# Optimization experiments

Measured on AMD Instinct MI355X. Metric: run time of the kernel, lower is better.

Reference implementation:

```python
import jax, jax.numpy as jnp
import numpy as np

N_NODES = 100000


def _add_self_loops(edge_index, n):
    loop = jnp.arange(n, dtype=edge_index.dtype)
    src = jnp.concatenate([edge_index[0], loop])
    dst = jnp.concatenate([edge_index[1], loop])
    return src, dst


def _gcn_conv(x, W, b, src, dst, n):
    # h = X W, then symmetric-normalized scatter-add over edges (PyG GCNConv)
    h = x @ W
    ones = jnp.ones(src.shape[0], dtype=h.dtype)
    deg = jax.ops.segment_sum(ones, dst, num_segments=n)  # in-degree incl. self loops
    dinv = jnp.where(deg > 0, jax.lax.rsqrt(deg), 0.0)
    norm = dinv[src] * dinv[dst]                           # [E]
    msg = h[src] * norm[:, None]                           # gather + scale
    out = jax.ops.segment_sum(msg, dst, num_segments=n)    # scatter-add
    return out + b


def setup_inputs() -> dict:
    key = jax.random.key(0)
    k1, k2, k3, k4 = jax.random.split(key, 4)
    F, H, C = 128, 128, 16
    x = jax.random.normal(k1, (N_NODES, F), dtype=jnp.float32)
    edge_index = jax.random.randint(k2, (2, 1600000), 0, N_NODES, dtype=jnp.int64)
    W1 = jax.random.normal(k3, (F, H), dtype=jnp.float32) / np.sqrt(F)
    b1 = jnp.zeros((H,), dtype=jnp.float32)
    W2 = jax.random.normal(k4, (H, C), dtype=jnp.float32) / np.sqrt(H)
    b2 = jnp.zeros((C,), dtype=jnp.float32)
    return {"x": x, "edge_index": edge_index, "W1": W1, "b1": b1, "W2": W2, "b2": b2}


def reference(x, edge_index, W1, b1, W2, b2):
    n = x.shape[0]
    src, dst = _add_self_loops(edge_index, n)
    h = _gcn_conv(x, W1, b1, src, dst, n)
    h = jax.nn.relu(h)
    # dropout(p=0.1) treated as identity (deterministic eval-mode reference)
    logits = _gcn_conv(h, W2, b2, src, dst, n)
    return logits, jax.nn.log_softmax(logits, axis=1)
```

## Files before the change

### kernel.cpp

```cpp
#include <hip/hip_runtime.h>
#include <math.h>


#define ELLW 72
#define EPB 16384
#define BSH 9
#define MAXEB 100
#define MAXBK 200

typedef __attribute__((ext_vector_type(8))) short short8;
typedef __attribute__((ext_vector_type(4))) float f32x4;

__device__ __forceinline__ float bf2f(unsigned short u) {
    return __uint_as_float(((unsigned int)u) << 16);
}
__device__ __forceinline__ unsigned short f2bf(float f) {
    unsigned int u = __float_as_uint(f);
    unsigned int r = (u + 0x7fffu + ((u >> 16) & 1u)) >> 16;
    return (unsigned short)r;
}

__global__ void k_prep(unsigned short* __restrict__ h, float* __restrict__ g,
                       const float* __restrict__ W1, unsigned short* __restrict__ wt,
                       int n) {
    int i = blockIdx.x * blockDim.x + threadIdx.x;
    if (i < 16384) {
        int nc = i >> 7, k = i & 127;
        wt[i] = f2bf(W1[k * 128 + nc]);
    }
    if (i < 128) h[(size_t)n * 128 + i] = 0;
    if (i < 16) g[(size_t)n * 16 + i] = 0.f;
}

__global__ void k_hist(const int* __restrict__ dst, int E,
                       int* __restrict__ hist, int nbuck) {
    __shared__ int lh[MAXBK];
    const int t = threadIdx.x, blk = blockIdx.x;
    for (int i = t; i < nbuck; i += 256) lh[i] = 0;
    __syncthreads();
    const int e0 = blk * EPB;
    const int e1 = min(e0 + EPB, E);
    for (int e = e0 + t; e < e1; e += 256)
        atomicAdd(&lh[dst[e] >> BSH], 1);
    __syncthreads();
    for (int i = t; i < nbuck; i += 256)
        hist[blk * nbuck + i] = lh[i];
}

__global__ void k_scan(int* __restrict__ hist, int* __restrict__ bstart,
                       int* __restrict__ bcount, int neb, int nbuck) {
    __shared__ unsigned short lh[MAXEB * MAXBK];
    __shared__ int sc[256];
    const int t = threadIdx.x;
    const int items = neb * nbuck;
    for (int i = t; i < items; i += 256) lh[i] = (unsigned short)hist[i];
    __syncthreads();
    int total = 0;
    if (t < nbuck)
        for (int blk = 0; blk < neb; ++blk) total += lh[blk * nbuck + t];
    sc[t] = total;
    __syncthreads();
    for (int o = 1; o < 256; o <<= 1) {
        int x = 0;
        if (t >= o) x = sc[t - o];
        __syncthreads();
        if (t >= o) sc[t] += x;
        __syncthreads();
    }
    if (t < nbuck) {
        int run = sc[t] - total;
        bstart[t] = run;
        bcount[t] = total;
        for (int blk = 0; blk < neb; ++blk) {
            int idx = blk * nbuck + t;
            int v = lh[idx];
            hist[idx] = run;
            run += v;
        }
    }
}

__global__ void k_bin(const int* __restrict__ src, const int* __restrict__ dst, int E,
                      const int* __restrict__ hist, int* __restrict__ binned, int nbuck) {
    __shared__ int cnt[MAXBK];
    const int t = threadIdx.x, blk = blockIdx.x;
    for (int i = t; i < nbuck; i += 256) cnt[i] = hist[blk * nbuck + i];
    __syncthreads();
    const int e0 = blk * EPB;
    const int e1 = min(e0 + EPB, E);
    for (int e = e0 + t; e < e1; e += 256) {
        int d = dst[e];
        int b = d >> BSH;
        int pos = atomicAdd(&cnt[b], 1);
        binned[pos] = src[e] | ((d & ((1 << BSH) - 1)) << 17);
    }
}

__global__ void k_ell(const int* __restrict__ binned, const int* __restrict__ bstart,
                      const int* __restrict__ bcount, int* __restrict__ deg,
                      int* __restrict__ col, int n) {
    __shared__ int ldeg[1 << BSH];
    const int t = threadIdx.x, b = blockIdx.x;
    const int node0 = b << BSH;
    for (int i = t; i < (1 << BSH); i += 256) ldeg[i] = 0;
    __syncthreads();
    const int st = bstart[b], cv = bcount[b];
    for (int i = t; i < cv; i += 256) {
        int v = binned[st + i];
        int s = v & 0x1FFFF;
        int dl = v >> 17;
        int q = atomicAdd(&ldeg[dl], 1);
        if (q < ELLW) col[(size_t)(node0 + dl) * ELLW + q] = s;
    }
    __syncthreads();
    for (int i = t; i < (1 << BSH); i += 256) {
        int node = node0 + i;
        if (node < n) {
            int dgv = ldeg[i];
            deg[node] = dgv;
            int dc = dgv > ELLW ? ELLW : dgv;
            int kend = (dc + 7) & ~7;
            for (int q = dc; q < kend; ++q) col[(size_t)node * ELLW + q] = n;
        }
    }
}

__global__ void k_gemm1(const float* __restrict__ x, const unsigned short* __restrict__ wt,
                        const int* __restrict__ deg, unsigned short* __restrict__ h,
                        int n) {
    __shared__ unsigned short xs[64 * 136];
    const int t = threadIdx.x;
    const int row0 = blockIdx.x * 64;
    for (int i = t; i < 2048; i += 256) {
        int r = i >> 5, c4 = (i & 31) << 2;
        int gr = row0 + r;
        float4 v = make_float4(0.f, 0.f, 0.f, 0.f);
        if (gr < n) v = *(const float4*)(x + (size_t)gr * 128 + c4);
        ushort4 u;
        u.x = f2bf(v.x); u.y = f2bf(v.y); u.z = f2bf(v.z); u.w = f2bf(v.w);
        *(ushort4*)(xs + r * 136 + c4) = u;
    }
    __syncthreads();
    const int w = t >> 6;
    const int lane = t & 63;
    const int m = lane & 15, q = lane >> 4;
    f32x4 acc[8];
#pragma unroll
    for (int ns = 0; ns < 8; ++ns) acc[ns] = (f32x4){0.f, 0.f, 0.f, 0.f};
#pragma unroll
    for (int kt = 0; kt < 4; ++kt) {
        short8 a = *(const short8*)(xs + (w * 16 + m) * 136 + kt * 32 + q * 8);
#pragma unroll
        for (int ns = 0; ns < 8; ++ns) {
            short8 b = *(const short8*)((const short*)wt + (ns * 16 + m) * 128 + kt * 32 + q * 8);
            acc[ns] = __builtin_amdgcn_mfma_f32_16x16x32_bf16(a, b, acc[ns], 0, 0, 0);
        }
    }
    unsigned short* xsw = xs + (w * 16) * 136;
    float srow[4];
#pragma unroll
    for (int reg = 0; reg < 4; ++reg) {
        int gr = row0 + w * 16 + q * 4 + reg;
        srow[reg] = (gr < n) ? rsqrtf((float)(deg[gr] + 1)) : 0.f;
    }
#pragma unroll
    for (int ns = 0; ns < 8; ++ns)
#pragma unroll
        for (int reg = 0; reg < 4; ++reg)
            xsw[(q * 4 + reg) * 136 + ns * 16 + m] = f2bf(acc[ns][reg] * srow[reg]);
    __syncthreads();
#pragma unroll
    for (int it = 0; it < 8; ++it) {
        int rl = (lane >> 5) + it * 2;
        int off = (lane & 31) * 4;
        int gr = row0 + w * 16 + rl;
        if (gr < n)
            *(ushort4*)(h + (size_t)gr * 128 + off) = *(const ushort4*)(xsw + rl * 136 + off);
    }
}

__global__ __launch_bounds__(256, 2) void k_gather1f(
        const unsigned short* __restrict__ h, const int* __restrict__ deg,
        const int* __restrict__ col, const float* __restrict__ b1,
        const float* __restrict__ W2, float* __restrict__ g, int n) {
    const int t = threadIdx.x;
    const int lane = t & 15;
    const int d = blockIdx.x * 16 + (t >> 4);
    if (d >= n) return;
    int dg = deg[d];
    if (dg > ELLW) dg = ELLW;
    const float dd = rsqrtf((float)(dg + 1));
    const int kend = (dg + 7) & ~7;
    const int* ecol = col + (size_t)d * ELLW;

    float aA[8], aB[8];
    {
        short8 u = *(const short8*)(h + (size_t)d * 128 + lane * 8);
#pragma unroll
        for (int j = 0; j < 8; ++j) {
            aA[j] = bf2f((unsigned short)u[j]);
            aB[j] = 0.f;
        }
    }
    for (int k = 0; k < kend; k += 8) {
        int4 c0 = *(const int4*)(ecol + k);
        int4 c1 = *(const int4*)(ecol + k + 4);
        short8 u0 = *(const short8*)(h + (size_t)c0.x * 128 + lane * 8);
        short8 u1 = *(const short8*)(h + (size_t)c0.y * 128 + lane * 8);
        short8 u2 = *(const short8*)(h + (size_t)c0.z * 128 + lane * 8);
        short8 u3 = *(const short8*)(h + (size_t)c0.w * 128 + lane * 8);
        short8 u4 = *(const short8*)(h + (size_t)c1.x * 128 + lane * 8);
        short8 u5 = *(const short8*)(h + (size_t)c1.y * 128 + lane * 8);
        short8 u6 = *(const short8*)(h + (size_t)c1.z * 128 + lane * 8);
        short8 u7 = *(const short8*)(h + (size_t)c1.w * 128 + lane * 8);
#pragma unroll
        for (int j = 0; j < 8; ++j) {
            aA[j] += bf2f((unsigned short)u0[j]) + bf2f((unsigned short)u2[j]) +
                     bf2f((unsigned short)u4[j]) + bf2f((unsigned short)u6[j]);
            aB[j] += bf2f((unsigned short)u1[j]) + bf2f((unsigned short)u3[j]) +
                     bf2f((unsigned short)u5[j]) + bf2f((unsigned short)u7[j]);
        }
    }
    float y[8];
    const float* b1p = b1 + lane * 8;
#pragma unroll
    for (int j = 0; j < 8; ++j)
        y[j] = fmaxf(fmaf(aA[j] + aB[j], dd, b1p[j]), 0.f);
    const float4* w2v = (const float4*)(W2 + lane * 8 * 16);
    float4 z0 = make_float4(0.f, 0.f, 0.f, 0.f);
    float4 z1 = z0, z2 = z0, z3 = z0;
#pragma unroll
    for (int j = 0; j < 8; ++j) {
        float4 w0 = w2v[j * 4 + 0], w1 = w2v[j * 4 + 1];
        float4 w2 = w2v[j * 4 + 2], w3 = w2v[j * 4 + 3];
        float yj = y[j];
        z0.x = fmaf(yj, w0.x, z0.x); z0.y = fmaf(yj, w0.y, z0.y);
        z0.z = fmaf(yj, w0.z, z0.z); z0.w = fmaf(yj, w0.w, z0.w);
        z1.x = fmaf(yj, w1.x, z1.x); z1.y = fmaf(yj, w1.y, z1.y);
        z1.z = fmaf(yj, w1.z, z1.z); z1.w = fmaf(yj, w1.w, z1.w);
        z2.x = fmaf(yj, w2.x, z2.x); z2.y = fmaf(yj, w2.y, z2.y);
        z2.z = fmaf(yj, w2.z, z2.z); z2.w = fmaf(yj, w2.w, z2.w);
        z3.x = fmaf(yj, w3.x, z3.x); z3.y = fmaf(yj, w3.y, z3.y);
        z3.z = fmaf(yj, w3.z, z3.z); z3.w = fmaf(yj, w3.w, z3.w);
    }
#pragma unroll
    for (int mm = 1; mm < 16; mm <<= 1) {
        z0.x += __shfl_xor(z0.x, mm); z0.y += __shfl_xor(z0.y, mm);
        z0.z += __shfl_xor(z0.z, mm); z0.w += __shfl_xor(z0.w, mm);
        z1.x += __shfl_xor(z1.x, mm); z1.y += __shfl_xor(z1.y, mm);
        z1.z += __shfl_xor(z1.z, mm); z1.w += __shfl_xor(z1.w, mm);
        z2.x += __shfl_xor(z2.x, mm); z2.y += __shfl_xor(z2.y, mm);
        z2.z += __shfl_xor(z2.z, mm); z2.w += __shfl_xor(z2.w, mm);
        z3.x += __shfl_xor(z3.x, mm); z3.y += __shfl_xor(z3.y, mm);
        z3.z += __shfl_xor(z3.z, mm); z3.w += __shfl_xor(z3.w, mm);
    }
    if (lane < 4) {
        float4 z = (lane == 0) ? z0 : (lane == 1) ? z1 : (lane == 2) ? z2 : z3;
        z.x *= dd; z.y *= dd; z.z *= dd; z.w *= dd;
        *(float4*)(g + (size_t)d * 16 + lane * 4) = z;
    }
}

#define FACC(acc, v) \
    acc.x += v.x; acc.y += v.y; acc.z += v.z; acc.w += v.w

__global__ void k_gather2(const float* __restrict__ g, const int* __restrict__ deg,
                          const int* __restrict__ col, const float* __restrict__ b2,
                          float* __restrict__ out, int n) {
    const int t = threadIdx.x;
    const int d = blockIdx.x * 64 + (t >> 2);
    if (d >= n) return;
    const int l = t & 3;
    int dg = deg[d];
    if (dg > ELLW) dg = ELLW;
    const float dd = rsqrtf((float)(dg + 1));
    const int kend = (dg + 7) & ~7;
    const int* ecol = col + (size_t)d * ELLW;

    float4 aA = *(const float4*)(g + (size_t)d * 16 + l * 4);
    float4 aB = make_float4(0.f, 0.f, 0.f, 0.f);
    float4 aC = aB, aD = aB;
    for (int k = 0; k < kend; k += 8) {
        int4 c0 = *(const int4*)(ecol + k);
        int4 c1 = *(const int4*)(ecol + k + 4);
        float4 h0 = *(const float4*)(g + (size_t)c0.x * 16 + l * 4);
        float4 h1 = *(const float4*)(g + (size_t)c0.y * 16 + l * 4);
        float4 h2 = *(const float4*)(g + (size_t)c0.z * 16 + l * 4);
        float4 h3 = *(const float4*)(g + (size_t)c0.w * 16 + l * 4);
        float4 h4 = *(const float4*)(g + (size_t)c1.x * 16 + l * 4);
        float4 h5 = *(const float4*)(g + (size_t)c1.y * 16 + l * 4);
        float4 h6 = *(const float4*)(g + (size_t)c1.z * 16 + l * 4);
        float4 h7 = *(const float4*)(g + (size_t)c1.w * 16 + l * 4);
        FACC(aA, h0); FACC(aB, h1); FACC(aC, h2); FACC(aD, h3);
        FACC(aA, h4); FACC(aB, h5); FACC(aC, h6); FACC(aD, h7);
    }
    float4 bv = *(const float4*)(b2 + l * 4);
    float4 acc;
    acc.x = fmaf(aA.x + aB.x + aC.x + aD.x, dd, bv.x);
    acc.y = fmaf(aA.y + aB.y + aC.y + aD.y, dd, bv.y);
    acc.z = fmaf(aA.z + aB.z + aC.z + aD.z, dd, bv.z);
    acc.w = fmaf(aA.w + aB.w + aC.w + aD.w, dd, bv.w);
    *(float4*)(out + (size_t)d * 16 + l * 4) = acc;
    float m = fmaxf(fmaxf(acc.x, acc.y), fmaxf(acc.z, acc.w));
    m = fmaxf(m, __shfl_xor(m, 1));
    m = fmaxf(m, __shfl_xor(m, 2));
    float e = expf(acc.x - m) + expf(acc.y - m) + expf(acc.z - m) + expf(acc.w - m);
    e += __shfl_xor(e, 1);
    e += __shfl_xor(e, 2);
    float ls = m + logf(e);
    float4 o;
    o.x = acc.x - ls; o.y = acc.y - ls; o.z = acc.z - ls; o.w = acc.w - ls;
    *(float4*)(out + (size_t)n * 16 + (size_t)d * 16 + l * 4) = o;
}

static inline size_t align256(size_t v) { return (v + 255) & ~(size_t)255; }

extern "C" void kernel_launch(void* const* d_in, const int* in_sizes, int n_in,
                              void* d_out, int out_size, void* d_ws, size_t ws_size,
                              hipStream_t stream) {
    const float* x  = (const float*)d_in[0];
    const int*   ei = (const int*)d_in[1];
    const float* W1 = (const float*)d_in[2];
    const float* b1 = (const float*)d_in[3];
    const float* W2 = (const float*)d_in[4];
    const float* b2 = (const float*)d_in[5];
    float* out = (float*)d_out;

    const int n = in_sizes[0] / 128;
    const int E = in_sizes[1] / 2;
    const int* src = ei;
    const int* dst = ei + E;
    const int NEB = (E + EPB - 1) / EPB;
    const int NBUCK = (n + (1 << BSH) - 1) >> BSH;

    char* base = (char*)d_ws;
    size_t off = 0;
    int* deg = (int*)(base + off); off = align256(off + (size_t)n * 4);
    int* col = (int*)(base + off); off = align256(off + (size_t)n * ELLW * 4);
    unsigned short* wt = (unsigned short*)(base + off); off = align256(off + 128 * 128 * 2);
    unsigned short* h = (unsigned short*)(base + off); off = align256(off + ((size_t)n + 1) * 128 * 2);
    float* g = (float*)(base + off); off = align256(off + ((size_t)n + 1) * 16 * 4);
    int* hist = (int*)(base + off); off = align256(off + (size_t)MAXEB * MAXBK * 4);
    int* bstart = (int*)(base + off); off = align256(off + (size_t)MAXBK * 4);
    int* bcount = (int*)(base + off); off = align256(off + (size_t)MAXBK * 4);
    int* binned = (int*)(base + off); off = align256(off + (size_t)E * 4);

    k_prep<<<64, 256, 0, stream>>>(h, g, W1, wt, n);
    k_hist<<<NEB, 256, 0, stream>>>(dst, E, hist, NBUCK);
    k_scan<<<1, 256, 0, stream>>>(hist, bstart, bcount, NEB, NBUCK);
    k_bin<<<NEB, 256, 0, stream>>>(src, dst, E, hist, binned, NBUCK);
    k_ell<<<NBUCK, 256, 0, stream>>>(binned, bstart, bcount, deg, col, n);

    k_gemm1<<<(n + 63) / 64, 256, 0, stream>>>(x, wt, deg, h, n);
    k_gather1f<<<(n + 15) / 16, 256, 0, stream>>>(h, deg, col, b1, W2, g, n);

    k_gather2<<<(n + 63) / 64, 256, 0, stream>>>(g, deg, col, b2, out, n);
}
```

Measured before the change: 360.2 us.

## Sort nodes by degree bucket and unroll gathers to sixteen neighbors

Adds a counting-sort pass (histogram, scan, place) that builds a permutation grouping nodes by padded degree, so the warps of a wavefront handle nodes with similar neighbor counts and waste fewer idle lanes. Both gather kernels index through this permutation, unroll the neighbor loop to 16 loads per iteration with four accumulators, and raise launch bounds to 3 blocks per CU. The cost is three extra small kernel launches plus a serial single-block scan, less locality in the output writes, and more register pressure from the deeper unroll.

```diff
diff --git a/kernel.cpp b/kernel.cpp
--- a/kernel.cpp
+++ b/kernel.cpp
@@ -7,6 +7,8 @@
 #define BSH 9
 #define MAXEB 100
 #define MAXBK 200
+#define NDB 10
+#define MAXNB 400
 
 typedef __attribute__((ext_vector_type(8))) short short8;
 typedef __attribute__((ext_vector_type(4))) float f32x4;
@@ -122,6 +124,65 @@
             int kend = (dc + 7) & ~7;
             for (int q = dc; q < kend; ++q) col[(size_t)node * ELLW + q] = n;
         }
+    }
+}
+
+__device__ __forceinline__ int kend_of(int dgv) {
+    int dc = dgv > ELLW ? ELLW : dgv;
+    return (dc + 7) & ~7;
+}
+
+__global__ void k_nhist(const int* __restrict__ deg, int* __restrict__ nhist, int n) {
+    __shared__ int lh[NDB];
+    const int t = threadIdx.x, blk = blockIdx.x;
+    if (t < NDB) lh[t] = 0;
+    __syncthreads();
+    int node = blk * 256 + t;
+    if (node < n) atomicAdd(&lh[kend_of(deg[node]) >> 3], 1);
+    __syncthreads();
+    if (t < NDB) nhist[blk * NDB + t] = lh[t];
+}
+
+__global__ void k_nscan(int* __restrict__ nhist, int nblk) {
+    __shared__ int lh[MAXNB * NDB];
+    __shared__ int tot[NDB], basev[NDB];
+    const int t = threadIdx.x;
+    const int items = nblk * NDB;
+    for (int i = t; i < items; i += 256) lh[i] = nhist[i];
+    __syncthreads();
+    if (t < NDB) {
+        int s = 0;
+        for (int blk = 0; blk < nblk; ++blk) s += lh[blk * NDB + t];
+        tot[t] = s;
+    }
+    __syncthreads();
+    if (t == 0) {
+        int run = 0;
+        for (int b = 0; b < NDB; ++b) { basev[b] = run; run += tot[b]; }
+    }
+    __syncthreads();
+    if (t < NDB) {
+        int run = basev[t];
+        for (int blk = 0; blk < nblk; ++blk) {
+            int idx = blk * NDB + t;
+            int v = lh[idx];
+            nhist[idx] = run;
+            run += v;
+        }
+    }
+}
+
+__global__ void k_nplace(const int* __restrict__ deg, const int* __restrict__ nhist,
+                         int* __restrict__ perm, int n) {
+    __shared__ int lc[NDB];
+    const int t = threadIdx.x, blk = blockIdx.x;
+    if (t < NDB) lc[t] = nhist[blk * NDB + t];
+    __syncthreads();
+    int node = blk * 256 + t;
+    if (node < n) {
+        int b = kend_of(deg[node]) >> 3;
+        int pos = atomicAdd(&lc[b], 1);
+        perm[pos] = node;
     }
 }
 
@@ -179,53 +240,63 @@
     }
 }
 
-__global__ __launch_bounds__(256, 2) void k_gather1f(
+#define LD8(var, idx) short8 var = *(const short8*)(h + (size_t)(idx) * 128 + lane * 8)
+#define AC8(accv, u) \
+    _Pragma("unroll") for (int j = 0; j < 8; ++j) accv[j] += bf2f((unsigned short)u[j])
+
+__global__ __launch_bounds__(256, 3) void k_gather1f(
         const unsigned short* __restrict__ h, const int* __restrict__ deg,
-        const int* __restrict__ col, const float* __restrict__ b1,
-        const float* __restrict__ W2, float* __restrict__ g, int n) {
+        const int* __restrict__ col, const int* __restrict__ perm,
+        const float* __restrict__ b1, const float* __restrict__ W2,
+        float* __restrict__ g, int n) {
     const int t = threadIdx.x;
     const int lane = t & 15;
-    const int d = blockIdx.x * 16 + (t >> 4);
-    if (d >= n) return;
+    const int idx = blockIdx.x * 16 + (t >> 4);
+    if (idx >= n) return;
+    const int d = perm[idx];
     int dg = deg[d];
     if (dg > ELLW) dg = ELLW;
     const float dd = rsqrtf((float)(dg + 1));
     const int kend = (dg + 7) & ~7;
     const int* ecol = col + (size_t)d * ELLW;
 
-    float aA[8], aB[8];
+    float aA[8], aB[8], aC[8], aD[8];
     {
-        short8 u = *(const short8*)(h + (size_t)d * 128 + lane * 8);
+        LD8(u, d);
 #pragma unroll
         for (int j = 0; j < 8; ++j) {
             aA[j] = bf2f((unsigned short)u[j]);
-            aB[j] = 0.f;
+            aB[j] = 0.f; aC[j] = 0.f; aD[j] = 0.f;
         }
     }
-    for (int k = 0; k < kend; k += 8) {
+    int k = 0;
+    for (; k + 16 <= kend; k += 16) {
         int4 c0 = *(const int4*)(ecol + k);
         int4 c1 = *(const int4*)(ecol + k + 4);
-        short8 u0 = *(const short8*)(h + (size_t)c0.x * 128 + lane * 8);
-        short8 u1 = *(const short8*)(h + (size_t)c0.y * 128 + lane * 8);
-        short8 u2 = *(const short8*)(h + (size_t)c0.z * 128 + lane * 8);
-        short8 u3 = *(const short8*)(h + (size_t)c0.w * 128 + lane * 8);
-        short8 u4 = *(const short8*)(h + (size_t)c1.x * 128 + lane * 8);
-        short8 u5 = *(const short8*)(h + (size_t)c1.y * 128 + lane * 8);
-        short8 u6 = *(const short8*)(h + (size_t)c1.z * 128 + lane * 8);
-        short8 u7 = *(const short8*)(h + (size_t)c1.w * 128 + lane * 8);
-#pragma unroll
-        for (int j = 0; j < 8; ++j) {
-            aA[j] += bf2f((unsigned short)u0[j]) + bf2f((unsigned short)u2[j]) +
-                     bf2f((unsigned short)u4[j]) + bf2f((unsigned short)u6[j]);
-            aB[j] += bf2f((unsigned short)u1[j]) + bf2f((unsigned short)u3[j]) +
-                     bf2f((unsigned short)u5[j]) + bf2f((unsigned short)u7[j]);
-        }
+        int4 c2 = *(const int4*)(ecol + k + 8);
+        int4 c3 = *(const int4*)(ecol + k + 12);
+        LD8(u0, c0.x); LD8(u1, c0.y); LD8(u2, c0.z); LD8(u3, c0.w);
+        LD8(u4, c1.x); LD8(u5, c1.y); LD8(u6, c1.z); LD8(u7, c1.w);
+        LD8(v0, c2.x); LD8(v1, c2.y); LD8(v2, c2.z); LD8(v3, c2.w);
+        LD8(v4, c3.x); LD8(v5, c3.y); LD8(v6, c3.z); LD8(v7, c3.w);
+        AC8(aA, u0); AC8(aB, u1); AC8(aC, u2); AC8(aD, u3);
+        AC8(aA, u4); AC8(aB, u5); AC8(aC, u6); AC8(aD, u7);
+        AC8(aA, v0); AC8(aB, v1); AC8(aC, v2); AC8(aD, v3);
+        AC8(aA, v4); AC8(aB, v5); AC8(aC, v6); AC8(aD, v7);
+    }
+    if (k < kend) {
+        int4 c0 = *(const int4*)(ecol + k);
+        int4 c1 = *(const int4*)(ecol + k + 4);
+        LD8(u0, c0.x); LD8(u1, c0.y); LD8(u2, c0.z); LD8(u3, c0.w);
+        LD8(u4, c1.x); LD8(u5, c1.y); LD8(u6, c1.z); LD8(u7, c1.w);
+        AC8(aA, u0); AC8(aB, u1); AC8(aC, u2); AC8(aD, u3);
+        AC8(aA, u4); AC8(aB, u5); AC8(aC, u6); AC8(aD, u7);
     }
     float y[8];
     const float* b1p = b1 + lane * 8;
 #pragma unroll
     for (int j = 0; j < 8; ++j)
-        y[j] = fmaxf(fmaf(aA[j] + aB[j], dd, b1p[j]), 0.f);
+        y[j] = fmaxf(fmaf(aA[j] + aB[j] + aC[j] + aD[j], dd, b1p[j]), 0.f);
     const float4* w2v = (const float4*)(W2 + lane * 8 * 16);
     float4 z0 = make_float4(0.f, 0.f, 0.f, 0.f);
     float4 z1 = z0, z2 = z0, z3 = z0;
@@ -263,13 +334,16 @@
 
 #define FACC(acc, v) \
     acc.x += v.x; acc.y += v.y; acc.z += v.z; acc.w += v.w
-
-__global__ void k_gather2(const float* __restrict__ g, const int* __restrict__ deg,
-                          const int* __restrict__ col, const float* __restrict__ b2,
-                          float* __restrict__ out, int n) {
+#define GLD(var, idx) float4 var = *(const float4*)(g + (size_t)(idx) * 16 + l * 4)
+
+__global__ __launch_bounds__(256, 3) void k_gather2(
+        const float* __restrict__ g, const int* __restrict__ deg,
+        const int* __restrict__ col, const int* __restrict__ perm,
+        const float* __restrict__ b2, float* __restrict__ out, int n) {
     const int t = threadIdx.x;
-    const int d = blockIdx.x * 64 + (t >> 2);
-    if (d >= n) return;
+    const int idx = blockIdx.x * 64 + (t >> 2);
+    if (idx >= n) return;
+    const int d = perm[idx];
     const int l = t & 3;
     int dg = deg[d];
     if (dg > ELLW) dg = ELLW;
@@ -280,17 +354,26 @@
     float4 aA = *(const float4*)(g + (size_t)d * 16 + l * 4);
     float4 aB = make_float4(0.f, 0.f, 0.f, 0.f);
     float4 aC = aB, aD = aB;
-    for (int k = 0; k < kend; k += 8) {
+    int k = 0;
+    for (; k + 16 <= kend; k += 16) {
         int4 c0 = *(const int4*)(ecol + k);
         int4 c1 = *(const int4*)(ecol + k + 4);
-        float4 h0 = *(const float4*)(g + (size_t)c0.x * 16 + l * 4);
-        float4 h1 = *(const float4*)(g + (size_t)c0.y * 16 + l * 4);
-        float4 h2 = *(const float4*)(g + (size_t)c0.z * 16 + l * 4);
-        float4 h3 = *(const float4*)(g + (size_t)c0.w * 16 + l * 4);
-        float4 h4 = *(const float4*)(g + (size_t)c1.x * 16 + l * 4);
-        float4 h5 = *(const float4*)(g + (size_t)c1.y * 16 + l * 4);
-        float4 h6 = *(const float4*)(g + (size_t)c1.z * 16 + l * 4);
-        float4 h7 = *(const float4*)(g + (size_t)c1.w * 16 + l * 4);
+        int4 c2 = *(const int4*)(ecol + k + 8);
+        int4 c3 = *(const int4*)(ecol + k + 12);
+        GLD(h0, c0.x); GLD(h1, c0.y); GLD(h2, c0.z); GLD(h3, c0.w);
+        GLD(h4, c1.x); GLD(h5, c1.y); GLD(h6, c1.z); GLD(h7, c1.w);
+        GLD(p0, c2.x); GLD(p1, c2.y); GLD(p2, c2.z); GLD(p3, c2.w);
+        GLD(p4, c3.x); GLD(p5, c3.y); GLD(p6, c3.z); GLD(p7, c3.w);
+        FACC(aA, h0); FACC(aB, h1); FACC(aC, h2); FACC(aD, h3);
+        FACC(aA, h4); FACC(aB, h5); FACC(aC, h6); FACC(aD, h7);
+        FACC(aA, p0); FACC(aB, p1); FACC(aC, p2); FACC(aD, p3);
+        FACC(aA, p4); FACC(aB, p5); FACC(aC, p6); FACC(aD, p7);
+    }
+    if (k < kend) {
+        int4 c0 = *(const int4*)(ecol + k);
+        int4 c1 = *(const int4*)(ecol + k + 4);
+        GLD(h0, c0.x); GLD(h1, c0.y); GLD(h2, c0.z); GLD(h3, c0.w);
+        GLD(h4, c1.x); GLD(h5, c1.y); GLD(h6, c1.z); GLD(h7, c1.w);
         FACC(aA, h0); FACC(aB, h1); FACC(aC, h2); FACC(aD, h3);
         FACC(aA, h4); FACC(aB, h5); FACC(aC, h6); FACC(aD, h7);
     }
@@ -332,6 +415,7 @@
     const int* dst = ei + E;
     const int NEB = (E + EPB - 1) / EPB;
     const int NBUCK = (n + (1 << BSH) - 1) >> BSH;
+    const int NBN = (n + 255) / 256;
 
     char* base = (char*)d_ws;
     size_t off = 0;
@@ -344,6 +428,8 @@
     int* bstart = (int*)(base + off); off = align256(off + (size_t)MAXBK * 4);
     int* bcount = (int*)(base + off); off = align256(off + (size_t)MAXBK * 4);
     int* binned = (int*)(base + off); off = align256(off + (size_t)E * 4);
+    int* nhist = (int*)(base + off); off = align256(off + (size_t)MAXNB * NDB * 4);
+    int* perm = (int*)(base + off); off = align256(off + (size_t)n * 4);
 
     k_prep<<<64, 256, 0, stream>>>(h, g, W1, wt, n);
     k_hist<<<NEB, 256, 0, stream>>>(dst, E, hist, NBUCK);
@@ -351,8 +437,12 @@
     k_bin<<<NEB, 256, 0, stream>>>(src, dst, E, hist, binned, NBUCK);
     k_ell<<<NBUCK, 256, 0, stream>>>(binned, bstart, bcount, deg, col, n);
 
+    k_nhist<<<NBN, 256, 0, stream>>>(deg, nhist, n);
+    k_nscan<<<1, 256, 0, stream>>>(nhist, NBN);
+    k_nplace<<<NBN, 256, 0, stream>>>(deg, nhist, perm, n);
+
     k_gemm1<<<(n + 63) / 64, 256, 0, stream>>>(x, wt, deg, h, n);
-    k_gather1f<<<(n + 15) / 16, 256, 0, stream>>>(h, deg, col, b1, W2, g, n);
-
-    k_gather2<<<(n + 63) / 64, 256, 0, stream>>>(g, deg, col, b2, out, n);
-}
+    k_gather1f<<<(n + 15) / 16, 256, 0, stream>>>(h, deg, col, perm, b1, W2, g, n);
+
+    k_gather2<<<(n + 63) / 64, 256, 0, stream>>>(g, deg, col, perm, b2, out, n);
+}
```

Result: slower. 377.0 us (+4.7%).
